# Kernel tuning notes

Hardware: AMD Instinct MI355X
Metric: run time of the kernel (lower is better)

## Reference

```python
import jax, jax.numpy as jnp
import numpy as np

N, D, U, E, B = 8192, 1024, 512, 8, 8


def setup_inputs() -> dict:
    key = jax.random.key(0)
    ks = jax.random.split(key, 8)
    x = jax.random.normal(ks[0], (N, D), dtype=jnp.float32)
    # stacked per-expert parameters (Dense + KolmogorovLayer)
    W1 = jax.random.normal(ks[1], (E, D, U), dtype=jnp.float32) * 0.02
    b1 = jnp.zeros((E, U), dtype=jnp.float32)
    proj = jax.random.normal(ks[2], (E, U, U), dtype=jnp.float32) * 0.02
    ctrl = jax.random.normal(ks[3], (E, B, U), dtype=jnp.float32) * 0.1
    scaling = jnp.ones((E, U), dtype=jnp.float32)
    # gating Dense
    Wg = jax.random.normal(ks[4], (D, E), dtype=jnp.float32) * 0.02
    bg = jnp.zeros((E,), dtype=jnp.float32)
    return {"x": x, "W1": W1, "b1": b1, "proj": proj, "ctrl": ctrl,
            "scaling": scaling, "Wg": Wg, "bg": bg}


def reference(x, W1, b1, proj, ctrl, scaling, Wg, bg):
    num_bases = ctrl.shape[1]
    # expert Dense + swish: [E, N, U]
    h = jax.nn.swish(jnp.einsum('nd,edu->enu', x, W1) + b1[:, None, :])
    # KolmogorovLayer: projection -> sigmoid -> gaussian-RBF B-spline basis
    z = jnp.einsum('enu,euv->env', h, proj)
    xn = jax.nn.sigmoid(z)                                   # [E, N, U] in (0,1)
    knots = jnp.linspace(0.0, 1.0, num_bases)                # [B]
    dist = (xn[..., None] - knots) ** 2                      # [E, N, U, B]
    basis = jnp.exp(-dist / (2.0 * (1.0 / num_bases) ** 2))
    basis = basis / (jnp.sum(basis, axis=-1, keepdims=True) + 1e-6)
    # contract bases with control points per unit, then scale: [E, N, U]
    expert_out = jnp.einsum('enub,ebu->enu', basis, ctrl) * scaling[:, None, :]
    # gating (inference path): hard one-hot argmax of logits
    logits = x @ Wg + bg                                     # [N, E]
    gate = jax.nn.one_hot(jnp.argmax(logits, axis=-1), logits.shape[-1],
                          dtype=x.dtype)                     # [N, E]
    # weighted sum over experts -> [N, U]
    return jnp.einsum('enu,ne->nu', expert_out, gate)
```

## Files before the change

### kernel.cpp

```cpp
#include <hip/hip_runtime.h>
#include <hip/hip_bf16.h>
#include <stdint.h>

#define NTOK 8192
#define DDIM 1024
#define UDIM 512
#define NEXP 8
#define MT_MAX 136

typedef __attribute__((ext_vector_type(8))) short bf16x8;
typedef __attribute__((ext_vector_type(4))) float f32x4;


__device__ __forceinline__ unsigned short f2bf(float f) {
  unsigned int u = __float_as_uint(f);
  u += 0x7FFFu + ((u >> 16) & 1u);
  return (unsigned short)(u >> 16);
}

__device__ __forceinline__ void gload16(const void* g, void* lds) {
  __builtin_amdgcn_global_load_lds(
      (__attribute__((address_space(1))) void*)(uintptr_t)g,
      (__attribute__((address_space(3))) void*)(uint32_t)(uintptr_t)lds,
      16, 0, 0);
}


__global__ __launch_bounds__(256) void k_prep_pack(
    const float* __restrict__ x, const float* __restrict__ Wg,
    const float* __restrict__ bg, const float* __restrict__ W1,
    const float* __restrict__ proj, unsigned short* __restrict__ xbf,
    int* __restrict__ eidx, unsigned short* __restrict__ W1p,
    unsigned short* __restrict__ projp) {
  __shared__ __align__(16) char smem[8 * 1040 * 4];
  const int t = threadIdx.x;

  if (blockIdx.x < 2048) {
    float (*WgT)[1040] = (float(*)[1040])smem;
#pragma unroll
    for (int r = 0; r < 32; ++r)
      WgT[t & 7][r * 32 + (t >> 3)] = Wg[r * 256 + t];
    __syncthreads();

    const int lane = t & 63;
    const int n = (blockIdx.x << 2) + (t >> 6);
    const float* xr = x + (size_t)n * DDIM;
    unsigned short* xo = xbf + (size_t)n * DDIM;
    float acc[8] = {0.f, 0.f, 0.f, 0.f, 0.f, 0.f, 0.f, 0.f};
#pragma unroll
    for (int c = 0; c < 4; ++c) {
      const int d = c * 256 + lane * 4;
      const float4 xv = *(const float4*)(xr + d);
      ushort4 o;
      o.x = f2bf(xv.x); o.y = f2bf(xv.y); o.z = f2bf(xv.z); o.w = f2bf(xv.w);
      *(ushort4*)(xo + d) = o;
#pragma unroll
      for (int e = 0; e < 8; ++e) {
        const float4 wv = *(const float4*)(&WgT[e][d]);
        acc[e] = fmaf(xv.x, wv.x, acc[e]);
        acc[e] = fmaf(xv.y, wv.y, acc[e]);
        acc[e] = fmaf(xv.z, wv.z, acc[e]);
        acc[e] = fmaf(xv.w, wv.w, acc[e]);
      }
    }
#pragma unroll
    for (int e = 0; e < 8; ++e) {
#pragma unroll
      for (int o = 32; o > 0; o >>= 1) acc[e] += __shfl_xor(acc[e], o, 64);
    }
    if (lane == 0) {
      int best = 0;
      float bv = acc[0] + bg[0];
#pragma unroll
      for (int e2 = 1; e2 < 8; ++e2) {
        const float v = acc[e2] + bg[e2];
        if (v > bv) { bv = v; best = e2; }
      }
      eidx[n] = best;
    }
  } else {
    float (*tile)[65] = (float(*)[65])smem;
    const int id = blockIdx.x - 2048;
    const int c0 = (id & 7) << 6;
    const int r0 = ((id >> 3) & 15) << 6;
    const int z = id >> 7;
    const int R = (z < 8) ? DDIM : UDIM;
    if (r0 >= R) return;
    const float* src = (z < 8) ? (W1 + (size_t)z * DDIM * UDIM)
                               : (proj + (size_t)(z - 8) * UDIM * UDIM);
    unsigned short* dst = (z < 8) ? (W1p + (size_t)z * DDIM * UDIM)
                                  : (projp + (size_t)(z - 8) * UDIM * UDIM);
#pragma unroll
    for (int i = 0; i < 4; ++i) {
      const int ri = (t >> 4) + i * 16;
      const int ci = (t & 15) * 4;
      const float4 v = *(const float4*)(src + (size_t)(r0 + ri) * UDIM + c0 + ci);
      tile[ri][ci] = v.x; tile[ri][ci + 1] = v.y; tile[ri][ci + 2] = v.z; tile[ri][ci + 3] = v.w;
    }
    __syncthreads();
    const int cc = t >> 2, ch = t & 3;
#pragma unroll
    for (int j = 0; j < 2; ++j) {
      const int kt = (r0 >> 5) + j;
      union { bf16x8 v; unsigned short u[8]; } pk;
#pragma unroll
      for (int q = 0; q < 8; ++q) pk.u[q] = f2bf(tile[j * 32 + ch * 8 + q][cc]);
      *(bf16x8*)(dst + ((size_t)kt * UDIM + c0 + cc) * 32 + ch * 8) = pk.v;
    }
  }
}


__global__ __launch_bounds__(1024) void k_sort(const int* __restrict__ eidx,
                                               int* __restrict__ perm_p,
                                               int* __restrict__ tile_expert,
                                               int* __restrict__ tile_rowlim) {
  __shared__ int hist[8][1024];
  __shared__ int tbase[9];
  const int t = threadIdx.x;

  int my[8], c[8] = {0, 0, 0, 0, 0, 0, 0, 0};
#pragma unroll
  for (int i = 0; i < 8; ++i) {
    my[i] = eidx[t * 8 + i];
#pragma unroll
    for (int b = 0; b < 8; ++b) c[b] += (my[i] == b);
  }
#pragma unroll
  for (int b = 0; b < 8; ++b) hist[b][t] = c[b];
  __syncthreads();

  for (int off = 1; off < 1024; off <<= 1) {
    int v[8];
#pragma unroll
    for (int b = 0; b < 8; ++b) v[b] = (t >= off) ? hist[b][t - off] : 0;
    __syncthreads();
#pragma unroll
    for (int b = 0; b < 8; ++b) hist[b][t] += v[b];
    __syncthreads();
  }

  if (t == 0) {
    int run = 0;
    for (int e = 0; e < 8; ++e) { tbase[e] = run; run += (hist[e][1023] + 63) >> 6; }
    tbase[8] = run;
  }
  __syncthreads();

  int base[8];
#pragma unroll
  for (int b = 0; b < 8; ++b) base[b] = (tbase[b] << 6) + hist[b][t] - c[b];
#pragma unroll
  for (int b = 0; b < 8; ++b) {
    int p = base[b];
#pragma unroll
    for (int i = 0; i < 8; ++i)
      if (my[i] == b) perm_p[p++] = t * 8 + i;
  }

  if (t < MT_MAX) {
    int e = -1, rl = 0;
#pragma unroll
    for (int q = 0; q < 8; ++q) {
      if (t >= tbase[q] && t < tbase[q + 1]) {
        e = q;
        const int r = hist[q][1023] - (t - tbase[q]) * 64;
        rl = r < 64 ? r : 64;
      }
    }
    tile_expert[t] = e;
    tile_rowlim[t] = rl;
  }
}


__global__ __launch_bounds__(256) void k_gemm1(
    const unsigned short* __restrict__ xbf, const unsigned short* __restrict__ W1p,
    const float* __restrict__ b1, const int* __restrict__ perm_p,
    const int* __restrict__ tile_expert, const int* __restrict__ tile_rowlim,
    unsigned short* __restrict__ Hp) {
  __shared__ __align__(16) short Ab[2][64 * 32];
  __shared__ __align__(16) short Bb[2][64 * 32];
  __shared__ int rows_s[64];

  const int orig = blockIdx.x;
  const int wg = (orig & 7) * (MT_MAX * 8 / 8) + (orig >> 3);
  const int Mt = wg >> 3, Nt = wg & 7;
  const int e = tile_expert[Mt];
  if (e < 0) return;
  const int rowlim = tile_rowlim[Mt];

  const int t = threadIdx.x;
  const int w = t >> 6, wr = w >> 1, wc = w & 1;
  const int lane = t & 63, ln15 = lane & 15, g = lane >> 4;

  if (t < 64) rows_s[t] = perm_p[Mt * 64 + (t < rowlim ? t : 0)];
  __syncthreads();

  const int srow = t >> 2;
  const int sh = (t & 3) ^ ((srow >> 1) & 3);
  const unsigned short* arow = xbf + (size_t)rows_s[srow] * DDIM + sh * 8;
  const unsigned short* Bpan = W1p + ((size_t)e * 32 * UDIM + Nt * 64) * 32;

  auto stage = [&](int kt, int buf) {
    gload16(arow + kt * 32, (char*)Ab[buf] + (t & ~63) * 16);
    gload16(Bpan + (size_t)kt * UDIM * 32 + srow * 32 + sh * 8,
            (char*)Bb[buf] + (t & ~63) * 16);
  };

  f32x4 acc[2][2];
  const f32x4 z4 = {0.f, 0.f, 0.f, 0.f};
  acc[0][0] = z4; acc[0][1] = z4; acc[1][0] = z4; acc[1][1] = z4;

  stage(0, 0);
  __syncthreads();
  int cur = 0;
  for (int kt = 0; kt < 32; ++kt) {
    const int nb = cur ^ 1;
    if (kt < 31) stage(kt + 1, nb);
    bf16x8 af[2], bf_[2];
#pragma unroll
    for (int mt = 0; mt < 2; ++mt) {
      const int r = wr * 32 + mt * 16 + ln15;
      af[mt] = *(const bf16x8*)((const char*)Ab[cur] + r * 64 + (g ^ ((r >> 1) & 3)) * 16);
    }
#pragma unroll
    for (int nt = 0; nt < 2; ++nt) {
      const int c2 = wc * 32 + nt * 16 + ln15;
      bf_[nt] = *(const bf16x8*)((const char*)Bb[cur] + c2 * 64 + (g ^ ((c2 >> 1) & 3)) * 16);
    }
#pragma unroll
    for (int mt = 0; mt < 2; ++mt)
#pragma unroll
      for (int nt = 0; nt < 2; ++nt)
        acc[mt][nt] = __builtin_amdgcn_mfma_f32_16x16x32_bf16(af[mt], bf_[nt], acc[mt][nt], 0, 0, 0);
    __syncthreads();
    cur = nb;
  }

  float bv[2];
#pragma unroll
  for (int nt = 0; nt < 2; ++nt)
    bv[nt] = b1[e * UDIM + Nt * 64 + wc * 32 + nt * 16 + ln15];
#pragma unroll
  for (int mt = 0; mt < 2; ++mt) {
#pragma unroll
    for (int nt = 0; nt < 2; ++nt) {
      const int colg = Nt * 64 + wc * 32 + nt * 16 + ln15;
      unsigned short* hp = Hp + ((size_t)(Mt * 16 + (colg >> 5)) * 64) * 32 + (colg & 31);
#pragma unroll
      for (int r = 0; r < 4; ++r) {
        const int row = wr * 32 + mt * 16 + g * 4 + r;
        const float a = acc[mt][nt][r] + bv[nt];
        hp[(size_t)row * 32] = f2bf(a * __builtin_amdgcn_rcpf(1.f + __expf(-a)));
      }
    }
  }
}


__global__ __launch_bounds__(256) void k_gemm2(
    const unsigned short* __restrict__ Hp, const unsigned short* __restrict__ projp,
    const float* __restrict__ ctrl, const float* __restrict__ scaling,
    const int* __restrict__ perm_p, const int* __restrict__ tile_expert,
    const int* __restrict__ tile_rowlim, float* __restrict__ out) {
  __shared__ __align__(16) short Ab[2][64 * 32];
  __shared__ __align__(16) short Bb[2][64 * 32];
  __shared__ int tok_s[64];

  const int orig = blockIdx.x;
  const int wg = (orig & 7) * (MT_MAX * 8 / 8) + (orig >> 3);
  const int Mt = wg >> 3, Nt = wg & 7;
  const int e = tile_expert[Mt];
  if (e < 0) return;
  const int rowlim = tile_rowlim[Mt];

  const int t = threadIdx.x;
  const int w = t >> 6, wr = w >> 1, wc = w & 1;
  const int lane = t & 63, ln15 = lane & 15, g = lane >> 4;

  if (t < 64) tok_s[t] = perm_p[Mt * 64 + (t < rowlim ? t : 0)];
  __syncthreads();

  const int srow = t >> 2;
  const int sh = (t & 3) ^ ((srow >> 1) & 3);
  const unsigned short* Apan = Hp + ((size_t)Mt * 16 * 64) * 32;
  const unsigned short* Bpan = projp + ((size_t)e * 16 * UDIM + Nt * 64) * 32;

  auto stage = [&](int kt, int buf) {
    gload16(Apan + (size_t)kt * 64 * 32 + srow * 32 + sh * 8,
            (char*)Ab[buf] + (t & ~63) * 16);
    gload16(Bpan + (size_t)kt * UDIM * 32 + srow * 32 + sh * 8,
            (char*)Bb[buf] + (t & ~63) * 16);
  };

  f32x4 acc[2][2];
  const f32x4 z4 = {0.f, 0.f, 0.f, 0.f};
  acc[0][0] = z4; acc[0][1] = z4; acc[1][0] = z4; acc[1][1] = z4;

  stage(0, 0);
  __syncthreads();
  int cur = 0;
  for (int kt = 0; kt < 16; ++kt) {
    const int nb = cur ^ 1;
    if (kt < 15) stage(kt + 1, nb);
    bf16x8 af[2], bf_[2];
#pragma unroll
    for (int mt = 0; mt < 2; ++mt) {
      const int r = wr * 32 + mt * 16 + ln15;
      af[mt] = *(const bf16x8*)((const char*)Ab[cur] + r * 64 + (g ^ ((r >> 1) & 3)) * 16);
    }
#pragma unroll
    for (int nt = 0; nt < 2; ++nt) {
      const int c2 = wc * 32 + nt * 16 + ln15;
      bf_[nt] = *(const bf16x8*)((const char*)Bb[cur] + c2 * 64 + (g ^ ((c2 >> 1) & 3)) * 16);
    }
#pragma unroll
    for (int mt = 0; mt < 2; ++mt)
#pragma unroll
      for (int nt = 0; nt < 2; ++nt)
        acc[mt][nt] = __builtin_amdgcn_mfma_f32_16x16x32_bf16(af[mt], bf_[nt], acc[mt][nt], 0, 0, 0);
    __syncthreads();
    cur = nb;
  }

  const float M = 0.27086949f;
  float cv[2][8], sc[2];
#pragma unroll
  for (int nt = 0; nt < 2; ++nt) {
    const int colg = Nt * 64 + wc * 32 + nt * 16 + ln15;
    sc[nt] = scaling[e * UDIM + colg];
#pragma unroll
    for (int b = 0; b < 8; ++b) cv[nt][b] = ctrl[((size_t)e * 8 + b) * UDIM + colg];
  }
#pragma unroll
  for (int mt = 0; mt < 2; ++mt) {
#pragma unroll
    for (int r = 0; r < 4; ++r) {
      const int row = wr * 32 + mt * 16 + g * 4 + r;
      if (row < rowlim) {
        const int tok = tok_s[row];
#pragma unroll
        for (int nt = 0; nt < 2; ++nt) {
          const int colg = Nt * 64 + wc * 32 + nt * 16 + ln15;
          const float z = acc[mt][nt][r];
          const float xn = __builtin_amdgcn_rcpf(1.f + __expf(-z));
          float q = __expf(-32.f * xn * xn);
          float rr = __expf(xn * (64.f / 7.f) - (32.f / 49.f));
          float s = 0.f, dc = 0.f;
#pragma unroll
          for (int b = 0; b < 8; ++b) {
            s += q;
            dc = fmaf(q, cv[nt][b], dc);
            q *= rr;
            rr *= M;
          }
          out[(size_t)tok * UDIM + colg] = dc * __builtin_amdgcn_rcpf(s + 1e-6f) * sc[nt];
        }
      }
    }
  }
}


extern "C" void kernel_launch(void* const* d_in, const int* in_sizes, int n_in,
                              void* d_out, int out_size, void* d_ws, size_t ws_size,
                              hipStream_t stream) {
  const float* x       = (const float*)d_in[0];
  const float* W1      = (const float*)d_in[1];
  const float* b1      = (const float*)d_in[2];
  const float* proj    = (const float*)d_in[3];
  const float* ctrl    = (const float*)d_in[4];
  const float* scaling = (const float*)d_in[5];
  const float* Wg      = (const float*)d_in[6];
  const float* bg      = (const float*)d_in[7];
  float* out = (float*)d_out;
  char* ws = (char*)d_ws;

  int* eidx        = (int*)(ws + 0);
  int* perm_p      = (int*)(ws + 32768);
  int* tile_expert = (int*)(ws + 69632 + 64);
  int* tile_rowlim = (int*)(ws + 69632 + 640);
  unsigned short* W1p   = (unsigned short*)(ws + 131072);
  unsigned short* projp = (unsigned short*)(ws + 131072 + 8388608);
  unsigned short* Hp    = (unsigned short*)(ws + 131072 + 8388608 + 4194304);
  unsigned short* xbf   = (unsigned short*)(ws + 131072 + 8388608 + 4194304 + 9175040);

  k_prep_pack<<<4096, 256, 0, stream>>>(x, Wg, bg, W1, proj, xbf, eidx, W1p, projp);
  k_sort<<<1, 1024, 0, stream>>>(eidx, perm_p, tile_expert, tile_rowlim);
  k_gemm1<<<MT_MAX * 8, 256, 0, stream>>>(xbf, W1p, b1, perm_p,
                                          tile_expert, tile_rowlim, Hp);
  k_gemm2<<<MT_MAX * 8, 256, 0, stream>>>(Hp, projp, ctrl, scaling, perm_p,
                                          tile_expert, tile_rowlim, out);
}
```

Baseline: 66.83 us.

## Triple-buffer GEMM tiles with one barrier per step; wave-scan sort histogram

Both expert GEMM kernels move from double to triple buffering of LDS tiles. The loop now issues loads two steps ahead and waits with an explicit vmcnt plus a single barrier per iteration, replacing the two __syncthreads per step, so global-load latency is better hidden. The sort kernel's shared-memory Hillis-Steele prefix scan (ten barrier rounds) is replaced with wave shuffles plus a small per-wave total scan. The price is more LDS per block and hand-coded waitcnt logic that depends on exactly two loads per stage.

```diff
diff --git a/kernel.cpp b/kernel.cpp
--- a/kernel.cpp
+++ b/kernel.cpp
@@ -115,9 +115,11 @@
                                                int* __restrict__ perm_p,
                                                int* __restrict__ tile_expert,
                                                int* __restrict__ tile_rowlim) {
-  __shared__ int hist[8][1024];
+  __shared__ int wavetot[8][16];
+  __shared__ int tot[8];
   __shared__ int tbase[9];
   const int t = threadIdx.x;
+  const int lane = t & 63, wid = t >> 6;
 
   int my[8], c[8] = {0, 0, 0, 0, 0, 0, 0, 0};
 #pragma unroll
@@ -126,30 +128,46 @@
 #pragma unroll
     for (int b = 0; b < 8; ++b) c[b] += (my[i] == b);
   }
-#pragma unroll
-  for (int b = 0; b < 8; ++b) hist[b][t] = c[b];
+
+  int inc[8];
+#pragma unroll
+  for (int b = 0; b < 8; ++b) {
+    int v = c[b];
+#pragma unroll
+    for (int o = 1; o < 64; o <<= 1) {
+      const int u = __shfl_up(v, o, 64);
+      if (lane >= o) v += u;
+    }
+    inc[b] = v;
+  }
+  if (lane == 63) {
+#pragma unroll
+    for (int b = 0; b < 8; ++b) wavetot[b][wid] = inc[b];
+  }
   __syncthreads();
 
-  for (int off = 1; off < 1024; off <<= 1) {
-    int v[8];
-#pragma unroll
-    for (int b = 0; b < 8; ++b) v[b] = (t >= off) ? hist[b][t - off] : 0;
-    __syncthreads();
-#pragma unroll
-    for (int b = 0; b < 8; ++b) hist[b][t] += v[b];
-    __syncthreads();
-  }
-
+  if (t < 8) {
+    int run = 0;
+#pragma unroll
+    for (int w2 = 0; w2 < 16; ++w2) {
+      const int u = wavetot[t][w2];
+      wavetot[t][w2] = run;
+      run += u;
+    }
+    tot[t] = run;
+  }
+  __syncthreads();
   if (t == 0) {
     int run = 0;
-    for (int e = 0; e < 8; ++e) { tbase[e] = run; run += (hist[e][1023] + 63) >> 6; }
+    for (int e = 0; e < 8; ++e) { tbase[e] = run; run += (tot[e] + 63) >> 6; }
     tbase[8] = run;
   }
   __syncthreads();
 
   int base[8];
 #pragma unroll
-  for (int b = 0; b < 8; ++b) base[b] = (tbase[b] << 6) + hist[b][t] - c[b];
+  for (int b = 0; b < 8; ++b)
+    base[b] = (tbase[b] << 6) + wavetot[b][wid] + inc[b] - c[b];
 #pragma unroll
   for (int b = 0; b < 8; ++b) {
     int p = base[b];
@@ -164,7 +182,7 @@
     for (int q = 0; q < 8; ++q) {
       if (t >= tbase[q] && t < tbase[q + 1]) {
         e = q;
-        const int r = hist[q][1023] - (t - tbase[q]) * 64;
+        const int r = tot[q] - (t - tbase[q]) * 64;
         rl = r < 64 ? r : 64;
       }
     }
@@ -179,12 +197,12 @@
     const float* __restrict__ b1, const int* __restrict__ perm_p,
     const int* __restrict__ tile_expert, const int* __restrict__ tile_rowlim,
     unsigned short* __restrict__ Hp) {
-  __shared__ __align__(16) short Ab[2][64 * 32];
-  __shared__ __align__(16) short Bb[2][64 * 32];
+  __shared__ __align__(16) short Ab[3][64 * 32];
+  __shared__ __align__(16) short Bb[3][64 * 32];
   __shared__ int rows_s[64];
 
   const int orig = blockIdx.x;
-  const int wg = (orig & 7) * (MT_MAX * 8 / 8) + (orig >> 3);
+  const int wg = (orig & 7) * MT_MAX + (orig >> 3);
   const int Mt = wg >> 3, Nt = wg & 7;
   const int e = tile_expert[Mt];
   if (e < 0) return;
@@ -213,11 +231,16 @@
   acc[0][0] = z4; acc[0][1] = z4; acc[1][0] = z4; acc[1][1] = z4;
 
   stage(0, 0);
-  __syncthreads();
+  stage(1, 1);
+  const int NK = 32;
   int cur = 0;
-  for (int kt = 0; kt < 32; ++kt) {
-    const int nb = cur ^ 1;
-    if (kt < 31) stage(kt + 1, nb);
+  for (int kt = 0; kt < NK; ++kt) {
+    __builtin_amdgcn_sched_barrier(0);
+    if (kt + 1 < NK) asm volatile("s_waitcnt vmcnt(2)" ::: "memory");
+    else             asm volatile("s_waitcnt vmcnt(0)" ::: "memory");
+    __builtin_amdgcn_s_barrier();
+    __builtin_amdgcn_sched_barrier(0);
+
     bf16x8 af[2], bf_[2];
 #pragma unroll
     for (int mt = 0; mt < 2; ++mt) {
@@ -234,8 +257,9 @@
 #pragma unroll
       for (int nt = 0; nt < 2; ++nt)
         acc[mt][nt] = __builtin_amdgcn_mfma_f32_16x16x32_bf16(af[mt], bf_[nt], acc[mt][nt], 0, 0, 0);
-    __syncthreads();
-    cur = nb;
+
+    if (kt + 2 < NK) stage(kt + 2, (cur + 2) % 3);
+    cur = (cur + 1) % 3;
   }
 
   float bv[2];
@@ -264,12 +288,12 @@
     const float* __restrict__ ctrl, const float* __restrict__ scaling,
     const int* __restrict__ perm_p, const int* __restrict__ tile_expert,
     const int* __restrict__ tile_rowlim, float* __restrict__ out) {
-  __shared__ __align__(16) short Ab[2][64 * 32];
-  __shared__ __align__(16) short Bb[2][64 * 32];
+  __shared__ __align__(16) short Ab[3][64 * 32];
+  __shared__ __align__(16) short Bb[3][64 * 32];
   __shared__ int tok_s[64];
 
   const int orig = blockIdx.x;
-  const int wg = (orig & 7) * (MT_MAX * 8 / 8) + (orig >> 3);
+  const int wg = (orig & 7) * MT_MAX + (orig >> 3);
   const int Mt = wg >> 3, Nt = wg & 7;
   const int e = tile_expert[Mt];
   if (e < 0) return;
@@ -299,11 +323,16 @@
   acc[0][0] = z4; acc[0][1] = z4; acc[1][0] = z4; acc[1][1] = z4;
 
   stage(0, 0);
-  __syncthreads();
+  stage(1, 1);
+  const int NK = 16;
   int cur = 0;
-  for (int kt = 0; kt < 16; ++kt) {
-    const int nb = cur ^ 1;
-    if (kt < 15) stage(kt + 1, nb);
+  for (int kt = 0; kt < NK; ++kt) {
+    __builtin_amdgcn_sched_barrier(0);
+    if (kt + 1 < NK) asm volatile("s_waitcnt vmcnt(2)" ::: "memory");
+    else             asm volatile("s_waitcnt vmcnt(0)" ::: "memory");
+    __builtin_amdgcn_s_barrier();
+    __builtin_amdgcn_sched_barrier(0);
+
     bf16x8 af[2], bf_[2];
 #pragma unroll
     for (int mt = 0; mt < 2; ++mt) {
@@ -320,8 +349,9 @@
 #pragma unroll
       for (int nt = 0; nt < 2; ++nt)
         acc[mt][nt] = __builtin_amdgcn_mfma_f32_16x16x32_bf16(af[mt], bf_[nt], acc[mt][nt], 0, 0, 0);
-    __syncthreads();
-    cur = nb;
+
+    if (kt + 2 < NK) stage(kt + 2, (cur + 2) % 3);
+    cur = (cur + 1) % 3;
   }
 
   const float M = 0.27086949f;
```

Result: no change. 67.13 us (+0.4%).
